# Optimization experiments

Hardware: AMD Instinct MI355X
Metric: run time of the kernel (lower is better)

## Reference

```python
import jax, jax.numpy as jnp
import numpy as np

TEMP = 1.0
NUM_HEADS = 4


def tropical_linear(x, W, b, temperature=TEMP):
    # x: (..., in), W: (out, in), b: (out,)
    # y_i = T * logsumexp_j((W_ij + x_j)/T) + b_i  (soft tropical max-plus)
    z = W + x[..., None, :]                      # (..., out, in) broadcast tensor
    y = temperature * jax.nn.logsumexp(z / temperature, axis=-1)
    return y + b


def setup_inputs() -> dict:
    key = jax.random.key(0)
    ks = jax.random.split(key, 5)
    B, S, E = 32, 64, 256  # seq_len == head_dim (= E / num_heads) required by original code
    x = jax.random.normal(ks[0], (B, S, E), dtype=jnp.float32)
    mk = lambda k: 0.1 * jax.random.normal(k, (E, E), dtype=jnp.float32)
    zb = jnp.zeros((E,), dtype=jnp.float32)
    return {
        "x": x,
        "Wq": mk(ks[1]), "bq": zb,
        "Wk": mk(ks[2]), "bk": zb,
        "Wv": mk(ks[3]), "bv": zb,
        "Wo": mk(ks[4]), "bo": zb,
    }


def reference(x, Wq, bq, Wk, bk, Wv, bv, Wo, bo):
    B, S, E = x.shape
    H = NUM_HEADS
    D = E // H  # == S by construction (required by original matmul)

    q = tropical_linear(x, Wq, bq)  # (B,S,E)
    k = tropical_linear(x, Wk, bk)
    v = tropical_linear(x, Wv, bv)

    # (B,S,E) -> (B,H,S,D)
    split = lambda t: t.reshape(B, S, H, D).transpose(0, 2, 1, 3)
    q, k, v = split(q), split(k), split(v)

    # Original: (q.unsqueeze(-1) + k.unsqueeze(-2).transpose(-1,-2)).sum(-1)
    # Both operands are (B,H,S,D,1) -> scores == q + k elementwise, shape (B,H,S,D).
    scores = q + k
    attn = jax.nn.softmax(scores / TEMP, axis=-1)  # (B,H,S,D)

    # matmul (B,H,S,D) @ (B,H,S,D) valid since D == S
    out = jnp.einsum('bhsd,bhde->bhse', attn, v)   # (B,H,S,D)
    out = out.transpose(0, 2, 1, 3).reshape(B, S, E)
    return tropical_linear(out, Wo, bo)
```

## Files before the change

kernel.cpp:

```cpp
#include <hip/hip_runtime.h>

constexpr int ED = 256;
constexpr int SD = 64;
constexpr int BD = 32;
constexpr int NROWS = BD * SD;
constexpr int RB = 4;

typedef short short8 __attribute__((ext_vector_type(8)));
typedef float floatx4 __attribute__((ext_vector_type(4)));

__device__ inline unsigned short f2bf(float f) {
  unsigned u = __float_as_uint(f);
  return (unsigned short)((u + 0x7fffu + ((u >> 16) & 1u)) >> 16);
}
__device__ inline float bf2f(unsigned short b) {
  return __uint_as_float(((unsigned)b) << 16);
}

__global__ __launch_bounds__(256) void expT_swz_kernel(
    const float* __restrict__ Wq, const float* __restrict__ Wk,
    const float* __restrict__ Wv,
    unsigned short* __restrict__ EqS, unsigned short* __restrict__ EkS,
    unsigned short* __restrict__ EvS)
{
  int z = blockIdx.y;
  const float* W = (z == 0) ? Wq : (z == 1) ? Wk : Wv;
  unsigned short* out = (z == 0) ? EqS : (z == 1) ? EkS : EvS;
  int t = threadIdx.x;
  int n = blockIdx.x * 8 + (t >> 5), kl = t & 31;
#pragma unroll
  for (int kk = 0; kk < 8; ++kk) {
    float v = __expf(W[n * ED + 32 * kk + kl]);
    out[(kk * 256 + n) * 32 + kl] = f2bf(v);
  }
}

__global__ __launch_bounds__(256) void expT_o_kernel(
    const float* __restrict__ Wo, unsigned short* __restrict__ EoT)
{
  __shared__ float ta[32][33];
  int tx = threadIdx.x & 31, ty = threadIdx.x >> 5;
  int i0 = blockIdx.y * 32, j0 = blockIdx.x * 32;
#pragma unroll
  for (int r = 0; r < 4; r++)
    ta[ty + 8 * r][tx] = __expf(Wo[(i0 + ty + 8 * r) * ED + j0 + tx]);
  __syncthreads();
#pragma unroll
  for (int r = 0; r < 4; r++)
    EoT[(j0 + ty + 8 * r) * ED + i0 + tx] = f2bf(ta[tx][ty + 8 * r]);
}

__global__ __launch_bounds__(256, 4) void qkv_mfma_kernel(
    const float* __restrict__ x,
    const unsigned short* __restrict__ EqS, const unsigned short* __restrict__ EkS,
    const unsigned short* __restrict__ EvS,
    const float* __restrict__ bq, const float* __restrict__ bk,
    const float* __restrict__ bv,
    float* __restrict__ attn, float* __restrict__ vout)
{
  int t = threadIdx.x;
  int w = t >> 6, lane = t & 63;
  int mt = blockIdx.x >> 2, h = blockIdx.x & 3;
  int row0 = mt * 16;

  __shared__ unsigned short aswz[8 * 512];
  __shared__ float fbuf[3][16][65];
  __shared__ float Mrow[16];

#pragma unroll
  for (int i = 0; i < 4; ++i) {
    int r = 4 * w + i;
    float4 xv = *(const float4*)&x[(size_t)(row0 + r) * ED + lane * 4];
    float m = fmaxf(fmaxf(xv.x, xv.y), fmaxf(xv.z, xv.w));
#pragma unroll
    for (int off = 32; off > 0; off >>= 1) m = fmaxf(m, __shfl_xor(m, off));
    ushort4 pk;
    pk.x = f2bf(__expf(xv.x - m));
    pk.y = f2bf(__expf(xv.y - m));
    pk.z = f2bf(__expf(xv.z - m));
    pk.w = f2bf(__expf(xv.w - m));
    int k0 = lane * 4;
    int idx = (k0 >> 5) * 512 + ((k0 >> 3) & 3) * 128 + r * 8 + (k0 & 7);
    *(ushort4*)&aswz[idx] = pk;
    if (lane == 0) Mrow[r] = m;
  }
  __syncthreads();

  short8 afrag[8];
#pragma unroll
  for (int kk = 0; kk < 8; ++kk)
    afrag[kk] = *(const short8*)&aswz[kk * 512 + lane * 8];

  int bb = ((h * 64 + w * 16 + (lane & 15)) << 2) + (w >> 2, lane >> 4);
  bb = ((h * 64 + w * 16 + (lane & 15)) << 2) + (lane >> 4);
  const short8* BQ = (const short8*)EqS;
  const short8* BK = (const short8*)EkS;
  const short8* BV = (const short8*)EvS;
  floatx4 accq = {0.f, 0.f, 0.f, 0.f};
  floatx4 acck = {0.f, 0.f, 0.f, 0.f};
  floatx4 accv = {0.f, 0.f, 0.f, 0.f};
#pragma unroll
  for (int kk = 0; kk < 8; ++kk) {
    short8 bqf = BQ[kk * 1024 + bb];
    short8 bkf = BK[kk * 1024 + bb];
    short8 bvf = BV[kk * 1024 + bb];
    accq = __builtin_amdgcn_mfma_f32_16x16x32_bf16(afrag[kk], bqf, accq, 0, 0, 0);
    acck = __builtin_amdgcn_mfma_f32_16x16x32_bf16(afrag[kk], bkf, acck, 0, 0, 0);
    accv = __builtin_amdgcn_mfma_f32_16x16x32_bf16(afrag[kk], bvf, accv, 0, 0, 0);
  }

  {
    int c = w * 16 + (lane & 15);
    int rb = (lane >> 4) * 4;
#pragma unroll
    for (int reg = 0; reg < 4; ++reg) {
      fbuf[0][rb + reg][c] = accq[reg];
      fbuf[1][rb + reg][c] = acck[reg];
      fbuf[2][rb + reg][c] = accv[reg];
    }
  }
  __syncthreads();

  int cg = h * 64 + lane;
  float bqv = bq[cg], bkv = bk[cg], bvv = bv[cg];
#pragma unroll
  for (int i = 0; i < 4; ++i) {
    int r = 4 * w + i;
    float Mr = Mrow[r];
    float qv = Mr + __logf(fbuf[0][r][lane]) + bqv;
    float kv = Mr + __logf(fbuf[1][r][lane]) + bkv;
    float vv = Mr + __logf(fbuf[2][r][lane]) + bvv;
    vout[(size_t)(row0 + r) * ED + cg] = vv;
    float s = qv + kv;
    float sm = s;
#pragma unroll
    for (int off = 32; off > 0; off >>= 1) sm = fmaxf(sm, __shfl_xor(sm, off));
    float ex = __expf(s - sm);
    float den = ex;
#pragma unroll
    for (int off = 32; off > 0; off >>= 1) den += __shfl_xor(den, off);
    attn[(size_t)(row0 + r) * ED + cg] = ex / den;
  }
}

__global__ __launch_bounds__(1024, 8) void avo_kernel(
    const float* __restrict__ attn, const float* __restrict__ vbuf,
    const unsigned short* __restrict__ EoT, const float* __restrict__ bo,
    float* __restrict__ y)
{
  int tid = threadIdx.x;
  int wv = tid >> 6, lane = tid & 63;
  int g = tid >> 8, t = tid & 255;
  int b = blockIdx.x >> 4;
  int row0 = b * SD + (blockIdx.x & 15) * RB;

  __shared__ float att[RB][ED];
  __shared__ float part[RB][ED][4];
  __shared__ float eoT[ED][RB];
  __shared__ float red[RB][4];

  att[g][t] = attn[(size_t)(row0 + g) * ED + t];
  float vr[16];
#pragma unroll
  for (int d = 0; d < 16; ++d)
    vr[d] = vbuf[(size_t)(b * SD + 16 * g + d) * ED + t];
  __syncthreads();

  int h64 = (t >> 6) << 6;
  float acc[RB];
#pragma unroll
  for (int r = 0; r < RB; ++r) {
    const float4* ap = (const float4*)&att[r][h64 + 16 * g];
    float a = 0.f;
#pragma unroll
    for (int d4 = 0; d4 < 4; ++d4) {
      float4 a4 = ap[d4];
      a = fmaf(a4.x, vr[4 * d4 + 0], a);
      a = fmaf(a4.y, vr[4 * d4 + 1], a);
      a = fmaf(a4.z, vr[4 * d4 + 2], a);
      a = fmaf(a4.w, vr[4 * d4 + 3], a);
    }
    acc[r] = a;
  }
#pragma unroll
  for (int r = 0; r < RB; ++r) part[r][t][g] = acc[r];
  __syncthreads();

  float4 p4 = *(const float4*)part[g][t];
  float orow = (p4.x + p4.y) + (p4.z + p4.w);
  float m = orow;
#pragma unroll
  for (int off = 32; off > 0; off >>= 1) m = fmaxf(m, __shfl_xor(m, off));
  if (lane == 0) red[g][wv & 3] = m;
  __syncthreads();
  float M = fmaxf(fmaxf(red[g][0], red[g][1]), fmaxf(red[g][2], red[g][3]));
  eoT[t][g] = __expf(orow - M);
  __syncthreads();

  float acc2[RB] = {0, 0, 0, 0};
  const unsigned short* po = EoT + (size_t)(64 * g) * ED + t;
#pragma unroll 4
  for (int j = 0; j < 64; ++j) {
    float4 e4 = *(const float4*)eoT[64 * g + j];
    float wo = bf2f(po[j * ED]);
    acc2[0] = fmaf(wo, e4.x, acc2[0]);
    acc2[1] = fmaf(wo, e4.y, acc2[1]);
    acc2[2] = fmaf(wo, e4.z, acc2[2]);
    acc2[3] = fmaf(wo, e4.w, acc2[3]);
  }
  __syncthreads();
#pragma unroll
  for (int r = 0; r < RB; ++r) part[r][t][g] = acc2[r];
  __syncthreads();

  float4 f4 = *(const float4*)part[g][t];
  float f = (f4.x + f4.y) + (f4.z + f4.w);
  y[(size_t)(row0 + g) * ED + t] = M + __logf(f) + bo[t];
}

extern "C" void kernel_launch(void* const* d_in, const int* in_sizes, int n_in,
                              void* d_out, int out_size, void* d_ws, size_t ws_size,
                              hipStream_t stream) {
  const float* x  = (const float*)d_in[0];
  const float* Wq = (const float*)d_in[1];
  const float* bq = (const float*)d_in[2];
  const float* Wk = (const float*)d_in[3];
  const float* bk = (const float*)d_in[4];
  const float* Wv = (const float*)d_in[5];
  const float* bv = (const float*)d_in[6];
  const float* Wo = (const float*)d_in[7];
  const float* bo = (const float*)d_in[8];
  float* y = (float*)d_out;

  char* ws = (char*)d_ws;
  unsigned short* EqS = (unsigned short*)(ws);
  unsigned short* EkS = (unsigned short*)(ws + 131072);
  unsigned short* EvS = (unsigned short*)(ws + 262144);
  unsigned short* EoT = (unsigned short*)(ws + 393216);
  float* attn = (float*)(ws + 524288);
  float* vbuf = (float*)(ws + 524288 + (size_t)NROWS * ED * 4);

  expT_swz_kernel<<<dim3(32, 3), 256, 0, stream>>>(Wq, Wk, Wv, EqS, EkS, EvS);
  expT_o_kernel<<<dim3(8, 8), 256, 0, stream>>>(Wo, EoT);
  qkv_mfma_kernel<<<512, 256, 0, stream>>>(x, EqS, EkS, EvS, bq, bk, bv,
                                           attn, vbuf);
  avo_kernel<<<NROWS / RB, 1024, 0, stream>>>(attn, vbuf, EoT, bo, y);
}
```

Baseline: 96.04 us.

## Move attention-V and output tropical projection onto fp16 MFMA with swizzled intermediates

Replaces the scalar FMA avo kernel with an MFMA-based kernel that computes attn·V and the exp-domain output projection using 16x16x32 fp16 matrix instructions. The qkv kernel now writes attention weights and V as fp16 directly in the pre-swizzled fragment layouts the next kernel consumes, which halves intermediate traffic. The Wo exp/transpose kernel is folded into the swizzled exp kernel, and all exp-weight tables switch from bf16 to fp16 for extra mantissa precision. The risks are fp16 range limits on exp values and a much smaller grid of 128 blocks for the final stage.

```diff
diff --git a/kernel.cpp b/kernel.cpp
--- a/kernel.cpp
+++ b/kernel.cpp
@@ -4,50 +4,30 @@
 constexpr int SD = 64;
 constexpr int BD = 32;
 constexpr int NROWS = BD * SD;
-constexpr int RB = 4;
-
-typedef short short8 __attribute__((ext_vector_type(8)));
+
+typedef _Float16 half8 __attribute__((ext_vector_type(8)));
 typedef float floatx4 __attribute__((ext_vector_type(4)));
 
-__device__ inline unsigned short f2bf(float f) {
-  unsigned u = __float_as_uint(f);
-  return (unsigned short)((u + 0x7fffu + ((u >> 16) & 1u)) >> 16);
-}
-__device__ inline float bf2f(unsigned short b) {
-  return __uint_as_float(((unsigned)b) << 16);
+__device__ inline unsigned short f2h(float f) {
+  union { _Float16 h; unsigned short u; } c;
+  c.h = (_Float16)f;
+  return c.u;
 }
 
 __global__ __launch_bounds__(256) void expT_swz_kernel(
     const float* __restrict__ Wq, const float* __restrict__ Wk,
-    const float* __restrict__ Wv,
+    const float* __restrict__ Wv, const float* __restrict__ Wo,
     unsigned short* __restrict__ EqS, unsigned short* __restrict__ EkS,
-    unsigned short* __restrict__ EvS)
+    unsigned short* __restrict__ EvS, unsigned short* __restrict__ EoS)
 {
   int z = blockIdx.y;
-  const float* W = (z == 0) ? Wq : (z == 1) ? Wk : Wv;
-  unsigned short* out = (z == 0) ? EqS : (z == 1) ? EkS : EvS;
+  const float* W = (z == 0) ? Wq : (z == 1) ? Wk : (z == 2) ? Wv : Wo;
+  unsigned short* out = (z == 0) ? EqS : (z == 1) ? EkS : (z == 2) ? EvS : EoS;
   int t = threadIdx.x;
   int n = blockIdx.x * 8 + (t >> 5), kl = t & 31;
 #pragma unroll
-  for (int kk = 0; kk < 8; ++kk) {
-    float v = __expf(W[n * ED + 32 * kk + kl]);
-    out[(kk * 256 + n) * 32 + kl] = f2bf(v);
-  }
-}
-
-__global__ __launch_bounds__(256) void expT_o_kernel(
-    const float* __restrict__ Wo, unsigned short* __restrict__ EoT)
-{
-  __shared__ float ta[32][33];
-  int tx = threadIdx.x & 31, ty = threadIdx.x >> 5;
-  int i0 = blockIdx.y * 32, j0 = blockIdx.x * 32;
-#pragma unroll
-  for (int r = 0; r < 4; r++)
-    ta[ty + 8 * r][tx] = __expf(Wo[(i0 + ty + 8 * r) * ED + j0 + tx]);
-  __syncthreads();
-#pragma unroll
-  for (int r = 0; r < 4; r++)
-    EoT[(j0 + ty + 8 * r) * ED + i0 + tx] = f2bf(ta[tx][ty + 8 * r]);
+  for (int kk = 0; kk < 8; ++kk)
+    out[(kk * 256 + n) * 32 + kl] = f2h(__expf(W[n * ED + 32 * kk + kl]));
 }
 
 __global__ __launch_bounds__(256, 4) void qkv_mfma_kernel(
@@ -56,7 +36,7 @@
     const unsigned short* __restrict__ EvS,
     const float* __restrict__ bq, const float* __restrict__ bk,
     const float* __restrict__ bv,
-    float* __restrict__ attn, float* __restrict__ vout)
+    unsigned short* __restrict__ AS, unsigned short* __restrict__ VS)
 {
   int t = threadIdx.x;
   int w = t >> 6, lane = t & 63;
@@ -75,10 +55,10 @@
 #pragma unroll
     for (int off = 32; off > 0; off >>= 1) m = fmaxf(m, __shfl_xor(m, off));
     ushort4 pk;
-    pk.x = f2bf(__expf(xv.x - m));
-    pk.y = f2bf(__expf(xv.y - m));
-    pk.z = f2bf(__expf(xv.z - m));
-    pk.w = f2bf(__expf(xv.w - m));
+    pk.x = f2h(__expf(xv.x - m));
+    pk.y = f2h(__expf(xv.y - m));
+    pk.z = f2h(__expf(xv.z - m));
+    pk.w = f2h(__expf(xv.w - m));
     int k0 = lane * 4;
     int idx = (k0 >> 5) * 512 + ((k0 >> 3) & 3) * 128 + r * 8 + (k0 & 7);
     *(ushort4*)&aswz[idx] = pk;
@@ -86,27 +66,26 @@
   }
   __syncthreads();
 
-  short8 afrag[8];
+  half8 afrag[8];
 #pragma unroll
   for (int kk = 0; kk < 8; ++kk)
-    afrag[kk] = *(const short8*)&aswz[kk * 512 + lane * 8];
-
-  int bb = ((h * 64 + w * 16 + (lane & 15)) << 2) + (w >> 2, lane >> 4);
-  bb = ((h * 64 + w * 16 + (lane & 15)) << 2) + (lane >> 4);
-  const short8* BQ = (const short8*)EqS;
-  const short8* BK = (const short8*)EkS;
-  const short8* BV = (const short8*)EvS;
+    afrag[kk] = *(const half8*)&aswz[kk * 512 + lane * 8];
+
+  int bb = ((h * 64 + w * 16 + (lane & 15)) << 2) + (lane >> 4);
+  const half8* BQ = (const half8*)EqS;
+  const half8* BK = (const half8*)EkS;
+  const half8* BV = (const half8*)EvS;
   floatx4 accq = {0.f, 0.f, 0.f, 0.f};
   floatx4 acck = {0.f, 0.f, 0.f, 0.f};
   floatx4 accv = {0.f, 0.f, 0.f, 0.f};
 #pragma unroll
   for (int kk = 0; kk < 8; ++kk) {
-    short8 bqf = BQ[kk * 1024 + bb];
-    short8 bkf = BK[kk * 1024 + bb];
-    short8 bvf = BV[kk * 1024 + bb];
-    accq = __builtin_amdgcn_mfma_f32_16x16x32_bf16(afrag[kk], bqf, accq, 0, 0, 0);
-    acck = __builtin_amdgcn_mfma_f32_16x16x32_bf16(afrag[kk], bkf, acck, 0, 0, 0);
-    accv = __builtin_amdgcn_mfma_f32_16x16x32_bf16(afrag[kk], bvf, accv, 0, 0, 0);
+    half8 bqf = BQ[kk * 1024 + bb];
+    half8 bkf = BK[kk * 1024 + bb];
+    half8 bvf = BV[kk * 1024 + bb];
+    accq = __builtin_amdgcn_mfma_f32_16x16x32_f16(afrag[kk], bqf, accq, 0, 0, 0);
+    acck = __builtin_amdgcn_mfma_f32_16x16x32_f16(afrag[kk], bkf, acck, 0, 0, 0);
+    accv = __builtin_amdgcn_mfma_f32_16x16x32_f16(afrag[kk], bvf, accv, 0, 0, 0);
   }
 
   {
@@ -123,6 +102,10 @@
 
   int cg = h * 64 + lane;
   float bqv = bq[cg], bkv = bk[cg], bvv = bv[cg];
+  int b = row0 >> 6;
+  int mt16 = (row0 >> 4) & 3;
+  size_t asBase = (size_t)(((b * 4 + mt16) * 4) + h) * 1024
+                + (lane >> 5) * 512 + ((lane >> 3) & 3) * 128 + (lane & 7);
 #pragma unroll
   for (int i = 0; i < 4; ++i) {
     int r = 4 * w + i;
@@ -130,7 +113,9 @@
     float qv = Mr + __logf(fbuf[0][r][lane]) + bqv;
     float kv = Mr + __logf(fbuf[1][r][lane]) + bkv;
     float vv = Mr + __logf(fbuf[2][r][lane]) + bvv;
-    vout[(size_t)(row0 + r) * ED + cg] = vv;
+    int d = mt16 * 16 + r;
+    VS[(size_t)(b * 2 + (d >> 5)) * 8192 + cg * 32 + ((d >> 3) & 3) * 8 + (d & 7)]
+        = f2h(vv);
     float s = qv + kv;
     float sm = s;
 #pragma unroll
@@ -139,83 +124,102 @@
     float den = ex;
 #pragma unroll
     for (int off = 32; off > 0; off >>= 1) den += __shfl_xor(den, off);
-    attn[(size_t)(row0 + r) * ED + cg] = ex / den;
-  }
-}
-
-__global__ __launch_bounds__(1024, 8) void avo_kernel(
-    const float* __restrict__ attn, const float* __restrict__ vbuf,
-    const unsigned short* __restrict__ EoT, const float* __restrict__ bo,
+    AS[asBase + r * 8] = f2h(ex / den);
+  }
+}
+
+__global__ __launch_bounds__(256) void avo_mfma_kernel(
+    const unsigned short* __restrict__ AS, const unsigned short* __restrict__ VS,
+    const unsigned short* __restrict__ EoS, const float* __restrict__ bo,
     float* __restrict__ y)
 {
-  int tid = threadIdx.x;
-  int wv = tid >> 6, lane = tid & 63;
-  int g = tid >> 8, t = tid & 255;
-  int b = blockIdx.x >> 4;
-  int row0 = b * SD + (blockIdx.x & 15) * RB;
-
-  __shared__ float att[RB][ED];
-  __shared__ float part[RB][ED][4];
-  __shared__ float eoT[ED][RB];
-  __shared__ float red[RB][4];
-
-  att[g][t] = attn[(size_t)(row0 + g) * ED + t];
-  float vr[16];
-#pragma unroll
-  for (int d = 0; d < 16; ++d)
-    vr[d] = vbuf[(size_t)(b * SD + 16 * g + d) * ED + t];
-  __syncthreads();
-
-  int h64 = (t >> 6) << 6;
-  float acc[RB];
-#pragma unroll
-  for (int r = 0; r < RB; ++r) {
-    const float4* ap = (const float4*)&att[r][h64 + 16 * g];
-    float a = 0.f;
-#pragma unroll
-    for (int d4 = 0; d4 < 4; ++d4) {
-      float4 a4 = ap[d4];
-      a = fmaf(a4.x, vr[4 * d4 + 0], a);
-      a = fmaf(a4.y, vr[4 * d4 + 1], a);
-      a = fmaf(a4.z, vr[4 * d4 + 2], a);
-      a = fmaf(a4.w, vr[4 * d4 + 3], a);
+  int t = threadIdx.x, w = t >> 6, lane = t & 63;
+  int b = blockIdx.x >> 2, mt = blockIdx.x & 3;
+  int row0 = b * 64 + mt * 16;
+  int q = lane >> 4, nl = lane & 15;
+
+  __shared__ float obuf[16][260];
+  __shared__ unsigned short easwz[8 * 512];
+  __shared__ float Mrow[16];
+
+  const half8* AS8 = (const half8*)(AS + (size_t)(((b * 4 + mt) * 4) + w) * 1024);
+  const half8* VS8 = (const half8*)VS;
+  half8 af0 = AS8[lane], af1 = AS8[64 + lane];
+  floatx4 acc[4];
+#pragma unroll
+  for (int nt = 0; nt < 4; ++nt) acc[nt] = (floatx4){0.f, 0.f, 0.f, 0.f};
+#pragma unroll
+  for (int nt = 0; nt < 4; ++nt) {
+    int n = w * 64 + nt * 16 + nl;
+    half8 b0 = VS8[(size_t)(b * 2 + 0) * 1024 + n * 4 + q];
+    half8 b1 = VS8[(size_t)(b * 2 + 1) * 1024 + n * 4 + q];
+    acc[nt] = __builtin_amdgcn_mfma_f32_16x16x32_f16(af0, b0, acc[nt], 0, 0, 0);
+    acc[nt] = __builtin_amdgcn_mfma_f32_16x16x32_f16(af1, b1, acc[nt], 0, 0, 0);
+  }
+  int rb = q * 4;
+#pragma unroll
+  for (int nt = 0; nt < 4; ++nt)
+#pragma unroll
+    for (int reg = 0; reg < 4; ++reg)
+      obuf[rb + reg][w * 64 + nt * 16 + nl] = acc[nt][reg];
+  __syncthreads();
+
+#pragma unroll
+  for (int i = 0; i < 4; ++i) {
+    int r = 4 * w + i;
+    float4 o4 = *(const float4*)&obuf[r][lane * 4];
+    float m = fmaxf(fmaxf(o4.x, o4.y), fmaxf(o4.z, o4.w));
+#pragma unroll
+    for (int off = 32; off > 0; off >>= 1) m = fmaxf(m, __shfl_xor(m, off));
+    ushort4 pk;
+    pk.x = f2h(__expf(o4.x - m));
+    pk.y = f2h(__expf(o4.y - m));
+    pk.z = f2h(__expf(o4.z - m));
+    pk.w = f2h(__expf(o4.w - m));
+    int k0 = lane * 4;
+    int idx = (k0 >> 5) * 512 + ((k0 >> 3) & 3) * 128 + r * 8 + (k0 & 7);
+    *(ushort4*)&easwz[idx] = pk;
+    if (lane == 0) Mrow[r] = m;
+  }
+  __syncthreads();
+
+  half8 af2[8];
+#pragma unroll
+  for (int kk = 0; kk < 8; ++kk)
+    af2[kk] = *(const half8*)&easwz[kk * 512 + lane * 8];
+  const half8* BO = (const half8*)EoS;
+  floatx4 acc2[4];
+#pragma unroll
+  for (int nt = 0; nt < 4; ++nt) acc2[nt] = (floatx4){0.f, 0.f, 0.f, 0.f};
+#pragma unroll
+  for (int kk = 0; kk < 8; ++kk) {
+#pragma unroll
+    for (int nt = 0; nt < 4; ++nt) {
+      int n = w * 64 + nt * 16 + nl;
+      acc2[nt] = __builtin_amdgcn_mfma_f32_16x16x32_f16(
+          af2[kk], BO[kk * 1024 + n * 4 + q], acc2[nt], 0, 0, 0);
     }
-    acc[r] = a;
-  }
-#pragma unroll
-  for (int r = 0; r < RB; ++r) part[r][t][g] = acc[r];
-  __syncthreads();
-
-  float4 p4 = *(const float4*)part[g][t];
-  float orow = (p4.x + p4.y) + (p4.z + p4.w);
-  float m = orow;
-#pragma unroll
-  for (int off = 32; off > 0; off >>= 1) m = fmaxf(m, __shfl_xor(m, off));
-  if (lane == 0) red[g][wv & 3] = m;
-  __syncthreads();
-  float M = fmaxf(fmaxf(red[g][0], red[g][1]), fmaxf(red[g][2], red[g][3]));
-  eoT[t][g] = __expf(orow - M);
-  __syncthreads();
-
-  float acc2[RB] = {0, 0, 0, 0};
-  const unsigned short* po = EoT + (size_t)(64 * g) * ED + t;
-#pragma unroll 4
-  for (int j = 0; j < 64; ++j) {
-    float4 e4 = *(const float4*)eoT[64 * g + j];
-    float wo = bf2f(po[j * ED]);
-    acc2[0] = fmaf(wo, e4.x, acc2[0]);
-    acc2[1] = fmaf(wo, e4.y, acc2[1]);
-    acc2[2] = fmaf(wo, e4.z, acc2[2]);
-    acc2[3] = fmaf(wo, e4.w, acc2[3]);
-  }
-  __syncthreads();
-#pragma unroll
-  for (int r = 0; r < RB; ++r) part[r][t][g] = acc2[r];
-  __syncthreads();
-
-  float4 f4 = *(const float4*)part[g][t];
-  float f = (f4.x + f4.y) + (f4.z + f4.w);
-  y[(size_t)(row0 + g) * ED + t] = M + __logf(f) + bo[t];
+  }
+#pragma unroll
+  for (int nt = 0; nt < 4; ++nt)
+#pragma unroll
+    for (int reg = 0; reg < 4; ++reg)
+      obuf[rb + reg][w * 64 + nt * 16 + nl] = acc2[nt][reg];
+  __syncthreads();
+
+  float4 bo4 = *(const float4*)&bo[lane * 4];
+#pragma unroll
+  for (int i = 0; i < 4; ++i) {
+    int r = 4 * w + i;
+    float4 f4 = *(const float4*)&obuf[r][lane * 4];
+    float M = Mrow[r];
+    float4 y4;
+    y4.x = M + __logf(f4.x) + bo4.x;
+    y4.y = M + __logf(f4.y) + bo4.y;
+    y4.z = M + __logf(f4.z) + bo4.z;
+    y4.w = M + __logf(f4.w) + bo4.w;
+    *(float4*)&y[(size_t)(row0 + r) * ED + lane * 4] = y4;
+  }
 }
 
 extern "C" void kernel_launch(void* const* d_in, const int* in_sizes, int n_in,
@@ -236,13 +240,13 @@
   unsigned short* EqS = (unsigned short*)(ws);
   unsigned short* EkS = (unsigned short*)(ws + 131072);
   unsigned short* EvS = (unsigned short*)(ws + 262144);
-  unsigned short* EoT = (unsigned short*)(ws + 393216);
-  float* attn = (float*)(ws + 524288);
-  float* vbuf = (float*)(ws + 524288 + (size_t)NROWS * ED * 4);
-
-  expT_swz_kernel<<<dim3(32, 3), 256, 0, stream>>>(Wq, Wk, Wv, EqS, EkS, EvS);
-  expT_o_kernel<<<dim3(8, 8), 256, 0, stream>>>(Wo, EoT);
+  unsigned short* EoS = (unsigned short*)(ws + 393216);
+  unsigned short* AS  = (unsigned short*)(ws + 524288);
+  unsigned short* VS  = (unsigned short*)(ws + 524288 + 1048576);
+
+  expT_swz_kernel<<<dim3(32, 4), 256, 0, stream>>>(Wq, Wk, Wv, Wo,
+                                                   EqS, EkS, EvS, EoS);
   qkv_mfma_kernel<<<512, 256, 0, stream>>>(x, EqS, EkS, EvS, bq, bk, bv,
-                                           attn, vbuf);
-  avo_kernel<<<NROWS / RB, 1024, 0, stream>>>(attn, vbuf, EoT, bo, y);
-}
+                                           AS, VS);
+  avo_mfma_kernel<<<128, 256, 0, stream>>>(AS, VS, EoS, bo, y);
+}
```

Result: faster. 88.77 us (-7.6%).
